# Performance work log

Measured on AMD Instinct MI355X. Metric: run time of the kernel, lower is better.

Reference implementation:

```python
import jax, jax.numpy as jnp
import numpy as np

MEM_DIM = 256
MEM_SIZE = 2048
N = 32768
K1 = 10
K2 = 10
BN_EPS = 1e-5
LEAKY_SLOPE = 0.01


def setup_inputs() -> dict:
    key = jax.random.key(0)
    k_x, k_m1, k_m2 = jax.random.split(key, 3)
    stdv = 1.0 / np.sqrt(MEM_DIM)
    x = jax.random.normal(k_x, (N, MEM_DIM), dtype=jnp.float32)
    mem1 = jax.random.uniform(k_m1, (MEM_SIZE, MEM_DIM), dtype=jnp.float32, minval=-stdv, maxval=stdv)
    mem2 = jax.random.uniform(k_m2, (MEM_SIZE, MEM_DIM), dtype=jnp.float32, minval=-stdv, maxval=stdv)
    gamma1 = jnp.ones((MEM_DIM,), jnp.float32)
    beta1 = jnp.zeros((MEM_DIM,), jnp.float32)
    gamma2 = jnp.ones((MEM_DIM,), jnp.float32)
    beta2 = jnp.zeros((MEM_DIM,), jnp.float32)
    return {"x": x, "mem1": mem1, "mem2": mem2,
            "gamma1": gamma1, "beta1": beta1, "gamma2": gamma2, "beta2": beta2}


def _basic_unit(x, mem, k):
    # cosine similarity: (x @ M^T) / (||x|| * ||M||)  -> [N, mem_size]
    sim = (x @ mem.T) / (jnp.linalg.norm(x, axis=1, keepdims=True)
                         * jnp.linalg.norm(mem, axis=1)[None, :])
    S, I = jax.lax.top_k(sim, k)                      # [N, k]
    w = jax.nn.softmax(jax.nn.relu(S), axis=1)        # sparse addressing weights
    # gather memory rows and weighted-sum: einsum('abc,ab->ac')
    return jnp.einsum('nkd,nk->nd', mem[I], w)


def _batchnorm_train(x, gamma, beta):
    mu = jnp.mean(x, axis=0)
    var = jnp.var(x, axis=0)  # biased, as torch BatchNorm uses for normalization
    return gamma * (x - mu) / jnp.sqrt(var + BN_EPS) + beta


def _leaky_relu(x):
    return jnp.where(x >= 0, x, LEAKY_SLOPE * x)


def reference(x, mem1, mem2, gamma1, beta1, gamma2, beta2):
    h = _basic_unit(x, mem1, K1)
    h = _leaky_relu(_batchnorm_train(h, gamma1, beta1))
    h = _basic_unit(h, mem2, K2)
    h = _leaky_relu(_batchnorm_train(h, gamma2, beta2))
    return h
```

## Files before the change

kernel.cpp:

```cpp
#include <hip/hip_runtime.h>
#include <math.h>


#define NROWS 32768
#define DIM   256
#define MSIZE 2048
#define TK    10
#define BM    64
#define BN    256
#define KC    32
#define NKC   8
#define NCC   8
#define NTHR  512
#define BNEPS 1e-5f
#define SLOPE 0.01f

union UMem {
  float ms[2][KC][BN];
  struct {
    float tw[8][8][TK];
    int   tx[8][8][TK];
    float cs[8][BN];
    float cq[8][BN];
  } f;
};

#define INSERT(LI, V, XI)                                               \
  do {                                                                  \
    const float v_ = (V);                                               \
    if (v_ > tv[LI][TK-1]) {                                            \
      float t_ = v_; int x_ = (XI);                                     \
      _Pragma("unroll")                                                 \
      for (int p_ = 0; p_ < TK; ++p_) {                                 \
        const bool  sw_ = (t_ > tv[LI][p_]);                            \
        const float ov_ = tv[LI][p_]; const int ox_ = ti_[LI][p_];      \
        tv[LI][p_]  = sw_ ? t_ : ov_;  ti_[LI][p_] = sw_ ? x_ : ox_;    \
        t_ = sw_ ? ov_ : t_;  x_ = sw_ ? ox_ : x_;                      \
      }                                                                 \
    }                                                                   \
  } while (0)

__global__ void __launch_bounds__(NTHR, 1) unit_kernel(
    const float* __restrict__ X,
    const float* __restrict__ M,
    const float* __restrict__ Minv,
    float* __restrict__ H,
    float* __restrict__ csum, float* __restrict__ csq)
{
  __shared__ float xs[BM][DIM];
  __shared__ UMem u;

  const int  tid  = threadIdx.x;
  const int  w    = tid >> 6;
  const int  lane = tid & 63;
  const bool hi   = lane >= 32;
  const int  row0 = blockIdx.x * BM;

  #pragma unroll
  for (int p = 0; p < 8; ++p) {
    const int r = p * 8 + w;
    const float4 v = reinterpret_cast<const float4*>(X + (size_t)(row0 + r) * DIM)[lane];
    float s = v.x*v.x + v.y*v.y + v.z*v.z + v.w*v.w;
    #pragma unroll
    for (int m = 32; m >= 1; m >>= 1) s += __shfl_xor(s, m, 64);
    const float sc = 1.0f / sqrtf(s);
    const float4 o = {v.x*sc, v.y*sc, v.z*sc, v.w*sc};
    reinterpret_cast<float4*>(&xs[r][0])[lane] = o;
  }
  __syncthreads();

  float tv[4][TK]; int ti_[4][TK];
  #pragma unroll
  for (int i = 0; i < 4; ++i)
    #pragma unroll
    for (int p = 0; p < TK; ++p) { tv[i][p] = -INFINITY; ti_[i][p] = 0x7FFFFFFF; }

  const int kq = tid & 7;

  for (int cc = 0; cc < NCC; ++cc) {
    const int col0 = cc * BN;

    float mc[4]; const float4* msrc[4]; int sloc[4];
    #pragma unroll
    for (int p = 0; p < 4; ++p) {
      const int mloc = p * 64 + (tid >> 3);
      mc[p]   = Minv[col0 + mloc];
      msrc[p] = reinterpret_cast<const float4*>(M + (size_t)(col0 + mloc) * DIM) + kq;
      sloc[p] = mloc ^ (kq << 3);
    }

    float acc[8][4];
    #pragma unroll
    for (int i = 0; i < 8; ++i)
      #pragma unroll
      for (int j = 0; j < 4; ++j) acc[i][j] = 0.f;

    float4 g[4];
    #pragma unroll
    for (int p = 0; p < 4; ++p) g[p] = msrc[p][0];
    #pragma unroll
    for (int p = 0; p < 4; ++p) {
      u.ms[0][kq*4+0][sloc[p]] = g[p].x * mc[p];
      u.ms[0][kq*4+1][sloc[p]] = g[p].y * mc[p];
      u.ms[0][kq*4+2][sloc[p]] = g[p].z * mc[p];
      u.ms[0][kq*4+3][sloc[p]] = g[p].w * mc[p];
    }
    __syncthreads();

    for (int kc = 0; kc < NKC; ++kc) {
      const int cur = kc & 1;
      if (kc < NKC - 1) {
        #pragma unroll
        for (int p = 0; p < 4; ++p) g[p] = msrc[p][(kc + 1) * 8];
      }
      #pragma unroll
      for (int k4 = 0; k4 < KC/4; ++k4) {
        float4 a4[8];
        #pragma unroll
        for (int i = 0; i < 8; ++i)
          a4[i] = *reinterpret_cast<const float4*>(&xs[w*8 + i][kc*KC + k4*4]);
        const int bcol = (lane * 4) ^ (k4 << 3);
        #pragma unroll
        for (int j4 = 0; j4 < 4; ++j4) {
          const float4 b = *reinterpret_cast<const float4*>(&u.ms[cur][k4*4 + j4][bcol]);
          #pragma unroll
          for (int i = 0; i < 8; ++i) {
            const float a = reinterpret_cast<const float*>(&a4[i])[j4];
            acc[i][0] = fmaf(a, b.x, acc[i][0]);
            acc[i][1] = fmaf(a, b.y, acc[i][1]);
            acc[i][2] = fmaf(a, b.z, acc[i][2]);
            acc[i][3] = fmaf(a, b.w, acc[i][3]);
          }
        }
      }
      if (kc < NKC - 1) {
        const int nxt = cur ^ 1;
        #pragma unroll
        for (int p = 0; p < 4; ++p) {
          u.ms[nxt][kq*4+0][sloc[p]] = g[p].x * mc[p];
          u.ms[nxt][kq*4+1][sloc[p]] = g[p].y * mc[p];
          u.ms[nxt][kq*4+2][sloc[p]] = g[p].z * mc[p];
          u.ms[nxt][kq*4+3][sloc[p]] = g[p].w * mc[p];
        }
        __syncthreads();
      }
    }

    float gv[4][4];
    #pragma unroll
    for (int i = 0; i < 4; ++i)
      #pragma unroll
      for (int j = 0; j < 4; ++j) {
        const float give = hi ? acc[i][j] : acc[i+4][j];
        gv[i][j] = __shfl_xor(give, 32, 64);
      }
    const int ownc = col0 + lane * 4;
    const int gotc = col0 + (lane ^ 32) * 4;
    #pragma unroll
    for (int i = 0; i < 4; ++i) {
      #pragma unroll
      for (int j = 0; j < 4; ++j) {
        const float v = hi ? gv[i][j] : acc[i][j];
        INSERT(i, v, (hi ? gotc : ownc) + j);
      }
      #pragma unroll
      for (int j = 0; j < 4; ++j) {
        const float v = hi ? acc[i+4][j] : gv[i][j];
        INSERT(i, v, (hi ? ownc : gotc) + j);
      }
    }
  }
  __syncthreads();

  #pragma unroll
  for (int li = 0; li < 4; ++li) {
    float wv[TK]; int wx[TK];
    #pragma unroll
    for (int e = 0; e < TK; ++e) {
      float hv = tv[li][0]; int hx = ti_[li][0];
      #pragma unroll
      for (int m = 1; m <= 16; m <<= 1) {
        const float ov = __shfl_xor(hv, m, 64);
        const int   ox = __shfl_xor(hx, m, 64);
        const bool take = (ov > hv) || ((ov == hv) && (ox < hx));
        hv = take ? ov : hv; hx = take ? ox : hx;
      }
      wv[e] = hv; wx[e] = hx;
      if (ti_[li][0] == hx) {
        #pragma unroll
        for (int p = 0; p < TK-1; ++p) { tv[li][p] = tv[li][p+1]; ti_[li][p] = ti_[li][p+1]; }
        tv[li][TK-1] = -INFINITY; ti_[li][TK-1] = 0x7FFFFFFF;
      }
    }
    const float mx = fmaxf(wv[0], 0.f);
    float we[TK]; float ssum = 0.f;
    #pragma unroll
    for (int e = 0; e < TK; ++e) { we[e] = expf(fmaxf(wv[e], 0.f) - mx); ssum += we[e]; }
    const float winv = 1.0f / ssum;
    const int r8 = (hi ? 4 : 0) + li;
    if ((lane & 31) == 0) {
      #pragma unroll
      for (int e = 0; e < TK; ++e) { u.f.tw[w][r8][e] = we[e] * winv; u.f.tx[w][r8][e] = wx[e]; }
    }
  }
  __syncthreads();

  float cS[4] = {0,0,0,0}, cQ[4] = {0,0,0,0};
  #pragma unroll
  for (int r8 = 0; r8 < 8; ++r8) {
    float h0 = 0.f, h1 = 0.f, h2 = 0.f, h3 = 0.f;
    #pragma unroll
    for (int e = 0; e < TK; ++e) {
      const float we = u.f.tw[w][r8][e];
      const int   xe = u.f.tx[w][r8][e];
      const float4 mv = reinterpret_cast<const float4*>(M + (size_t)xe * DIM)[lane];
      h0 = fmaf(we, mv.x, h0); h1 = fmaf(we, mv.y, h1);
      h2 = fmaf(we, mv.z, h2); h3 = fmaf(we, mv.w, h3);
    }
    const int row = row0 + w*8 + r8;
    const float4 o = {h0, h1, h2, h3};
    reinterpret_cast<float4*>(H + (size_t)row * DIM)[lane] = o;
    cS[0] += h0; cS[1] += h1; cS[2] += h2; cS[3] += h3;
    cQ[0] = fmaf(h0,h0,cQ[0]); cQ[1] = fmaf(h1,h1,cQ[1]);
    cQ[2] = fmaf(h2,h2,cQ[2]); cQ[3] = fmaf(h3,h3,cQ[3]);
  }
  {
    const float4 s4 = {cS[0],cS[1],cS[2],cS[3]}, q4 = {cQ[0],cQ[1],cQ[2],cQ[3]};
    *reinterpret_cast<float4*>(&u.f.cs[w][lane*4]) = s4;
    *reinterpret_cast<float4*>(&u.f.cq[w][lane*4]) = q4;
  }
  __syncthreads();
  {
    const int col = tid & 255;
    float s = 0.f;
    if (tid < 256) {
      #pragma unroll
      for (int w8 = 0; w8 < 8; ++w8) s += u.f.cs[w8][col];
      atomicAdd(&csum[col], s);
    } else {
      #pragma unroll
      for (int w8 = 0; w8 < 8; ++w8) s += u.f.cq[w8][col];
      atomicAdd(&csq[col], s);
    }
  }
}

__global__ void __launch_bounds__(256) memnorm_kernel(
    const float* __restrict__ m1, const float* __restrict__ m2,
    float* __restrict__ inv1, float* __restrict__ inv2)
{
  const int row  = blockIdx.x * 4 + (threadIdx.x >> 6);
  const int lane = threadIdx.x & 63;
  const float* src = (row < MSIZE) ? m1 : m2;
  const int r = row & (MSIZE - 1);
  const float4 v = reinterpret_cast<const float4*>(src)[r * (DIM/4) + lane];
  float s = v.x*v.x + v.y*v.y + v.z*v.z + v.w*v.w;
  #pragma unroll
  for (int m = 32; m >= 1; m >>= 1) s += __shfl_xor(s, m, 64);
  if (lane == 0) ((row < MSIZE) ? inv1 : inv2)[r] = 1.0f / sqrtf(s);
}

__global__ void __launch_bounds__(256) bn_kernel(
    const float* __restrict__ in, float* __restrict__ out,
    const float* __restrict__ cs, const float* __restrict__ cq,
    const float* __restrict__ gam, const float* __restrict__ bet)
{
  const int tid = threadIdx.x;
  const int c0  = (tid & 63) * 4;
  const int ro  = tid >> 6;
  const float invN = 1.0f / (float)NROWS;
  float sc[4], sh[4];
  #pragma unroll
  for (int j = 0; j < 4; ++j) {
    const int c = c0 + j;
    const float mean = cs[c] * invN;
    const float var  = cq[c] * invN - mean * mean;
    const float s    = gam[c] / sqrtf(var + BNEPS);
    sc[j] = s; sh[j] = bet[c] - mean * s;
  }
  const int rbase = blockIdx.x * 128;
  #pragma unroll 4
  for (int it = 0; it < 32; ++it) {
    const int r = rbase + ro + it * 4;
    const float4 v = reinterpret_cast<const float4*>(in + (size_t)r * DIM)[tid & 63];
    float y0 = fmaf(sc[0], v.x, sh[0]);
    float y1 = fmaf(sc[1], v.y, sh[1]);
    float y2 = fmaf(sc[2], v.z, sh[2]);
    float y3 = fmaf(sc[3], v.w, sh[3]);
    y0 = y0 >= 0.f ? y0 : SLOPE * y0;
    y1 = y1 >= 0.f ? y1 : SLOPE * y1;
    y2 = y2 >= 0.f ? y2 : SLOPE * y2;
    y3 = y3 >= 0.f ? y3 : SLOPE * y3;
    const float4 o = {y0, y1, y2, y3};
    reinterpret_cast<float4*>(out + (size_t)r * DIM)[tid & 63] = o;
  }
}

extern "C" void kernel_launch(void* const* d_in, const int* in_sizes, int n_in,
                              void* d_out, int out_size, void* d_ws, size_t ws_size,
                              hipStream_t stream) {
  (void)in_sizes; (void)n_in; (void)out_size; (void)ws_size;
  const float* x    = (const float*)d_in[0];
  const float* mem1 = (const float*)d_in[1];
  const float* mem2 = (const float*)d_in[2];
  const float* g1   = (const float*)d_in[3];
  const float* b1   = (const float*)d_in[4];
  const float* g2   = (const float*)d_in[5];
  const float* b2   = (const float*)d_in[6];
  float* out = (float*)d_out;
  float* ws  = (float*)d_ws;

  float* minv1 = ws;
  float* minv2 = ws + 2048;
  float* cs1   = ws + 4096;
  float* cq1   = ws + 4352;
  float* cs2   = ws + 4608;
  float* cq2   = ws + 4864;

  memnorm_kernel<<<(2 * MSIZE) / 4, 256, 0, stream>>>(mem1, mem2, minv1, minv2);
  hipMemsetAsync(cs1, 0, 4 * 256 * sizeof(float), stream);

  unit_kernel<<<NROWS / BM, NTHR, 0, stream>>>(x, mem1, minv1, out, cs1, cq1);
  bn_kernel<<<NROWS / 128, 256, 0, stream>>>(out, out, cs1, cq1, g1, b1);
  unit_kernel<<<NROWS / BM, NTHR, 0, stream>>>(out, mem2, minv2, out, cs2, cq2);
  bn_kernel<<<NROWS / 128, 256, 0, stream>>>(out, out, cs2, cq2, g2, b2);
}
```

Baseline: 8.697 ms.

## Move BN stats out of unit kernel and target two waves per EU

Removes the per-block column sum and sum-of-squares reduction and its global atomics from the unit kernel, and replaces them with separate partial-sum and reduce kernels over the output. The unit kernel now uses amdgpu_waves_per_eu(2,2) in place of launch_bounds min-blocks 1, and its register-array loops are rewritten as explicit float4 scalars to help allocation. The intent is to cut LDS use and register pressure so two blocks can share a CU, at the cost of an extra full read of H and two extra launches per layer. Forcing two waves per EU may make the compiler spill registers.

```diff
diff --git a/kernel.cpp b/kernel.cpp
--- a/kernel.cpp
+++ b/kernel.cpp
@@ -12,6 +12,7 @@
 #define NKC   8
 #define NCC   8
 #define NTHR  512
+#define SBLK  128
 #define BNEPS 1e-5f
 #define SLOPE 0.01f
 
@@ -20,8 +21,6 @@
   struct {
     float tw[8][8][TK];
     int   tx[8][8][TK];
-    float cs[8][BN];
-    float cq[8][BN];
   } f;
 };
 
@@ -36,16 +35,34 @@
         const float ov_ = tv[LI][p_]; const int ox_ = ti_[LI][p_];      \
         tv[LI][p_]  = sw_ ? t_ : ov_;  ti_[LI][p_] = sw_ ? x_ : ox_;    \
         t_ = sw_ ? ov_ : t_;  x_ = sw_ ? ox_ : x_;                      \
-      }                                                                 \
+      }                                                                  \
     }                                                                   \
   } while (0)
 
-__global__ void __launch_bounds__(NTHR, 1) unit_kernel(
+#define FMA_ROW(ACC, AV)                                                \
+  ACC.x = fmaf((AV), b.x, ACC.x); ACC.y = fmaf((AV), b.y, ACC.y);       \
+  ACC.z = fmaf((AV), b.z, ACC.z); ACC.w = fmaf((AV), b.w, ACC.w);
+
+#define K4STEP(J4, COMP)                                                \
+  { const float4 b = *reinterpret_cast<const float4*>(&u.ms[cur][k4*4 + (J4)][bcol]); \
+    FMA_ROW(acc0, a_0.COMP) FMA_ROW(acc1, a_1.COMP)                     \
+    FMA_ROW(acc2, a_2.COMP) FMA_ROW(acc3, a_3.COMP)                     \
+    FMA_ROW(acc4, a_4.COMP) FMA_ROW(acc5, a_5.COMP)                     \
+    FMA_ROW(acc6, a_6.COMP) FMA_ROW(acc7, a_7.COMP) }
+
+#define STAGE1(BUF, G, MC, SL)                                          \
+  u.ms[BUF][kq*4+0][SL] = (G).x * (MC);                                 \
+  u.ms[BUF][kq*4+1][SL] = (G).y * (MC);                                 \
+  u.ms[BUF][kq*4+2][SL] = (G).z * (MC);                                 \
+  u.ms[BUF][kq*4+3][SL] = (G).w * (MC);
+
+__global__ void __launch_bounds__(NTHR)
+__attribute__((amdgpu_waves_per_eu(2, 2)))
+unit_kernel(
     const float* __restrict__ X,
     const float* __restrict__ M,
     const float* __restrict__ Minv,
-    float* __restrict__ H,
-    float* __restrict__ csum, float* __restrict__ csq)
+    float* __restrict__ H)
 {
   __shared__ float xs[BM][DIM];
   __shared__ UMem u;
@@ -75,100 +92,89 @@
     #pragma unroll
     for (int p = 0; p < TK; ++p) { tv[i][p] = -INFINITY; ti_[i][p] = 0x7FFFFFFF; }
 
-  const int kq = tid & 7;
+  const int kq   = tid & 7;
+  const int mrow = tid >> 3;
+  const int sl   = mrow ^ (kq << 3);
+  const int sloc0 = sl, sloc1 = 64 + sl, sloc2 = 128 + sl, sloc3 = 192 + sl;
 
   for (int cc = 0; cc < NCC; ++cc) {
     const int col0 = cc * BN;
 
-    float mc[4]; const float4* msrc[4]; int sloc[4];
-    #pragma unroll
-    for (int p = 0; p < 4; ++p) {
-      const int mloc = p * 64 + (tid >> 3);
-      mc[p]   = Minv[col0 + mloc];
-      msrc[p] = reinterpret_cast<const float4*>(M + (size_t)(col0 + mloc) * DIM) + kq;
-      sloc[p] = mloc ^ (kq << 3);
-    }
-
-    float acc[8][4];
-    #pragma unroll
-    for (int i = 0; i < 8; ++i)
-      #pragma unroll
-      for (int j = 0; j < 4; ++j) acc[i][j] = 0.f;
-
-    float4 g[4];
-    #pragma unroll
-    for (int p = 0; p < 4; ++p) g[p] = msrc[p][0];
-    #pragma unroll
-    for (int p = 0; p < 4; ++p) {
-      u.ms[0][kq*4+0][sloc[p]] = g[p].x * mc[p];
-      u.ms[0][kq*4+1][sloc[p]] = g[p].y * mc[p];
-      u.ms[0][kq*4+2][sloc[p]] = g[p].z * mc[p];
-      u.ms[0][kq*4+3][sloc[p]] = g[p].w * mc[p];
-    }
+    const float mc0 = Minv[col0 + mrow];
+    const float mc1 = Minv[col0 + 64 + mrow];
+    const float mc2 = Minv[col0 + 128 + mrow];
+    const float mc3 = Minv[col0 + 192 + mrow];
+    const float4* msrc0 = reinterpret_cast<const float4*>(M + (size_t)(col0 +        mrow) * DIM) + kq;
+    const float4* msrc1 = reinterpret_cast<const float4*>(M + (size_t)(col0 +  64 + mrow) * DIM) + kq;
+    const float4* msrc2 = reinterpret_cast<const float4*>(M + (size_t)(col0 + 128 + mrow) * DIM) + kq;
+    const float4* msrc3 = reinterpret_cast<const float4*>(M + (size_t)(col0 + 192 + mrow) * DIM) + kq;
+
+    float4 acc0 = {0,0,0,0}, acc1 = {0,0,0,0}, acc2 = {0,0,0,0}, acc3 = {0,0,0,0};
+    float4 acc4 = {0,0,0,0}, acc5 = {0,0,0,0}, acc6 = {0,0,0,0}, acc7 = {0,0,0,0};
+
+    float4 g0 = msrc0[0], g1 = msrc1[0], g2 = msrc2[0], g3 = msrc3[0];
+    STAGE1(0, g0, mc0, sloc0) STAGE1(0, g1, mc1, sloc1)
+    STAGE1(0, g2, mc2, sloc2) STAGE1(0, g3, mc3, sloc3)
     __syncthreads();
 
     for (int kc = 0; kc < NKC; ++kc) {
       const int cur = kc & 1;
       if (kc < NKC - 1) {
-        #pragma unroll
-        for (int p = 0; p < 4; ++p) g[p] = msrc[p][(kc + 1) * 8];
+        g0 = msrc0[(kc + 1) * 8]; g1 = msrc1[(kc + 1) * 8];
+        g2 = msrc2[(kc + 1) * 8]; g3 = msrc3[(kc + 1) * 8];
       }
       #pragma unroll
       for (int k4 = 0; k4 < KC/4; ++k4) {
-        float4 a4[8];
-        #pragma unroll
-        for (int i = 0; i < 8; ++i)
-          a4[i] = *reinterpret_cast<const float4*>(&xs[w*8 + i][kc*KC + k4*4]);
+        const int kbase = kc * KC + k4 * 4;
+        const float4 a_0 = *reinterpret_cast<const float4*>(&xs[w*8 + 0][kbase]);
+        const float4 a_1 = *reinterpret_cast<const float4*>(&xs[w*8 + 1][kbase]);
+        const float4 a_2 = *reinterpret_cast<const float4*>(&xs[w*8 + 2][kbase]);
+        const float4 a_3 = *reinterpret_cast<const float4*>(&xs[w*8 + 3][kbase]);
+        const float4 a_4 = *reinterpret_cast<const float4*>(&xs[w*8 + 4][kbase]);
+        const float4 a_5 = *reinterpret_cast<const float4*>(&xs[w*8 + 5][kbase]);
+        const float4 a_6 = *reinterpret_cast<const float4*>(&xs[w*8 + 6][kbase]);
+        const float4 a_7 = *reinterpret_cast<const float4*>(&xs[w*8 + 7][kbase]);
         const int bcol = (lane * 4) ^ (k4 << 3);
-        #pragma unroll
-        for (int j4 = 0; j4 < 4; ++j4) {
-          const float4 b = *reinterpret_cast<const float4*>(&u.ms[cur][k4*4 + j4][bcol]);
-          #pragma unroll
-          for (int i = 0; i < 8; ++i) {
-            const float a = reinterpret_cast<const float*>(&a4[i])[j4];
-            acc[i][0] = fmaf(a, b.x, acc[i][0]);
-            acc[i][1] = fmaf(a, b.y, acc[i][1]);
-            acc[i][2] = fmaf(a, b.z, acc[i][2]);
-            acc[i][3] = fmaf(a, b.w, acc[i][3]);
-          }
-        }
+        K4STEP(0, x) K4STEP(1, y) K4STEP(2, z) K4STEP(3, w)
       }
       if (kc < NKC - 1) {
         const int nxt = cur ^ 1;
-        #pragma unroll
-        for (int p = 0; p < 4; ++p) {
-          u.ms[nxt][kq*4+0][sloc[p]] = g[p].x * mc[p];
-          u.ms[nxt][kq*4+1][sloc[p]] = g[p].y * mc[p];
-          u.ms[nxt][kq*4+2][sloc[p]] = g[p].z * mc[p];
-          u.ms[nxt][kq*4+3][sloc[p]] = g[p].w * mc[p];
-        }
+        STAGE1(nxt, g0, mc0, sloc0) STAGE1(nxt, g1, mc1, sloc1)
+        STAGE1(nxt, g2, mc2, sloc2) STAGE1(nxt, g3, mc3, sloc3)
         __syncthreads();
       }
     }
 
-    float gv[4][4];
-    #pragma unroll
-    for (int i = 0; i < 4; ++i)
-      #pragma unroll
-      for (int j = 0; j < 4; ++j) {
-        const float give = hi ? acc[i][j] : acc[i+4][j];
-        gv[i][j] = __shfl_xor(give, 32, 64);
-      }
+    float4 gv0, gv1, gv2, gv3;
+    {
+      const float4 s0 = hi ? acc0 : acc4;
+      const float4 s1 = hi ? acc1 : acc5;
+      const float4 s2 = hi ? acc2 : acc6;
+      const float4 s3 = hi ? acc3 : acc7;
+      gv0.x = __shfl_xor(s0.x, 32, 64); gv0.y = __shfl_xor(s0.y, 32, 64);
+      gv0.z = __shfl_xor(s0.z, 32, 64); gv0.w = __shfl_xor(s0.w, 32, 64);
+      gv1.x = __shfl_xor(s1.x, 32, 64); gv1.y = __shfl_xor(s1.y, 32, 64);
+      gv1.z = __shfl_xor(s1.z, 32, 64); gv1.w = __shfl_xor(s1.w, 32, 64);
+      gv2.x = __shfl_xor(s2.x, 32, 64); gv2.y = __shfl_xor(s2.y, 32, 64);
+      gv2.z = __shfl_xor(s2.z, 32, 64); gv2.w = __shfl_xor(s2.w, 32, 64);
+      gv3.x = __shfl_xor(s3.x, 32, 64); gv3.y = __shfl_xor(s3.y, 32, 64);
+      gv3.z = __shfl_xor(s3.z, 32, 64); gv3.w = __shfl_xor(s3.w, 32, 64);
+    }
     const int ownc = col0 + lane * 4;
     const int gotc = col0 + (lane ^ 32) * 4;
-    #pragma unroll
-    for (int i = 0; i < 4; ++i) {
-      #pragma unroll
-      for (int j = 0; j < 4; ++j) {
-        const float v = hi ? gv[i][j] : acc[i][j];
-        INSERT(i, v, (hi ? gotc : ownc) + j);
-      }
-      #pragma unroll
-      for (int j = 0; j < 4; ++j) {
-        const float v = hi ? acc[i+4][j] : gv[i][j];
-        INSERT(i, v, (hi ? ownc : gotc) + j);
-      }
-    }
+    const int cA = hi ? gotc : ownc;
+    const int cB = hi ? ownc : gotc;
+    #define INS_LIST(LI, GVI, AI, AI4)                                   \
+      { const float4 fb = hi ? (GVI) : (AI); const float4 sb = hi ? (AI4) : (GVI); \
+        INSERT(LI, fb.x, cA+0); INSERT(LI, fb.y, cA+1);                  \
+        INSERT(LI, fb.z, cA+2); INSERT(LI, fb.w, cA+3);                  \
+        INSERT(LI, sb.x, cB+0); INSERT(LI, sb.y, cB+1);                  \
+        INSERT(LI, sb.z, cB+2); INSERT(LI, sb.w, cB+3); }
+    INS_LIST(0, gv0, acc0, acc4)
+    INS_LIST(1, gv1, acc1, acc5)
+    INS_LIST(2, gv2, acc2, acc6)
+    INS_LIST(3, gv3, acc3, acc7)
+    #undef INS_LIST
   }
   __syncthreads();
 
@@ -205,7 +211,6 @@
   }
   __syncthreads();
 
-  float cS[4] = {0,0,0,0}, cQ[4] = {0,0,0,0};
   #pragma unroll
   for (int r8 = 0; r8 < 8; ++r8) {
     float h0 = 0.f, h1 = 0.f, h2 = 0.f, h3 = 0.f;
@@ -220,28 +225,6 @@
     const int row = row0 + w*8 + r8;
     const float4 o = {h0, h1, h2, h3};
     reinterpret_cast<float4*>(H + (size_t)row * DIM)[lane] = o;
-    cS[0] += h0; cS[1] += h1; cS[2] += h2; cS[3] += h3;
-    cQ[0] = fmaf(h0,h0,cQ[0]); cQ[1] = fmaf(h1,h1,cQ[1]);
-    cQ[2] = fmaf(h2,h2,cQ[2]); cQ[3] = fmaf(h3,h3,cQ[3]);
-  }
-  {
-    const float4 s4 = {cS[0],cS[1],cS[2],cS[3]}, q4 = {cQ[0],cQ[1],cQ[2],cQ[3]};
-    *reinterpret_cast<float4*>(&u.f.cs[w][lane*4]) = s4;
-    *reinterpret_cast<float4*>(&u.f.cq[w][lane*4]) = q4;
-  }
-  __syncthreads();
-  {
-    const int col = tid & 255;
-    float s = 0.f;
-    if (tid < 256) {
-      #pragma unroll
-      for (int w8 = 0; w8 < 8; ++w8) s += u.f.cs[w8][col];
-      atomicAdd(&csum[col], s);
-    } else {
-      #pragma unroll
-      for (int w8 = 0; w8 < 8; ++w8) s += u.f.cq[w8][col];
-      atomicAdd(&csq[col], s);
-    }
   }
 }
 
@@ -258,6 +241,36 @@
   #pragma unroll
   for (int m = 32; m >= 1; m >>= 1) s += __shfl_xor(s, m, 64);
   if (lane == 0) ((row < MSIZE) ? inv1 : inv2)[r] = 1.0f / sqrtf(s);
+}
+
+__global__ void __launch_bounds__(256) stats_part_kernel(
+    const float* __restrict__ H, float* __restrict__ part)
+{
+  const int c = threadIdx.x;
+  const int b = blockIdx.x;
+  const int rows = NROWS / SBLK;
+  const float* p = H + (size_t)b * rows * DIM + c;
+  float s = 0.f, q = 0.f;
+  #pragma unroll 8
+  for (int r = 0; r < rows; ++r) {
+    const float v = p[(size_t)r * DIM];
+    s += v; q = fmaf(v, v, q);
+  }
+  part[(size_t)(b * 2 + 0) * DIM + c] = s;
+  part[(size_t)(b * 2 + 1) * DIM + c] = q;
+}
+
+__global__ void __launch_bounds__(512) stats_reduce_kernel(
+    const float* __restrict__ part, float* __restrict__ cs, float* __restrict__ cq)
+{
+  const int t  = threadIdx.x;
+  const int c  = t & 255;
+  const int sq = t >> 8;
+  float s = 0.f;
+  #pragma unroll 8
+  for (int b = 0; b < SBLK; ++b)
+    s += part[(size_t)(b * 2 + sq) * DIM + c];
+  (sq ? cq : cs)[c] = s;
 }
 
 __global__ void __launch_bounds__(256) bn_kernel(
@@ -312,16 +325,21 @@
 
   float* minv1 = ws;
   float* minv2 = ws + 2048;
-  float* cs1   = ws + 4096;
-  float* cq1   = ws + 4352;
-  float* cs2   = ws + 4608;
-  float* cq2   = ws + 4864;
+  float* part  = ws + 4096;
+  float* cs1   = ws + 4096 + SBLK * 2 * DIM;
+  float* cq1   = cs1 + 256;
+  float* cs2   = cq1 + 256;
+  float* cq2   = cs2 + 256;
 
   memnorm_kernel<<<(2 * MSIZE) / 4, 256, 0, stream>>>(mem1, mem2, minv1, minv2);
-  hipMemsetAsync(cs1, 0, 4 * 256 * sizeof(float), stream);
-
-  unit_kernel<<<NROWS / BM, NTHR, 0, stream>>>(x, mem1, minv1, out, cs1, cq1);
+
+  unit_kernel<<<NROWS / BM, NTHR, 0, stream>>>(x, mem1, minv1, out);
+  stats_part_kernel<<<SBLK, 256, 0, stream>>>(out, part);
+  stats_reduce_kernel<<<1, 512, 0, stream>>>(part, cs1, cq1);
   bn_kernel<<<NROWS / 128, 256, 0, stream>>>(out, out, cs1, cq1, g1, b1);
-  unit_kernel<<<NROWS / BM, NTHR, 0, stream>>>(out, mem2, minv2, out, cs2, cq2);
+
+  unit_kernel<<<NROWS / BM, NTHR, 0, stream>>>(out, mem2, minv2, out);
+  stats_part_kernel<<<SBLK, 256, 0, stream>>>(out, part);
+  stats_reduce_kernel<<<1, 512, 0, stream>>>(part, cs2, cq2);
   bn_kernel<<<NROWS / 128, 256, 0, stream>>>(out, out, cs2, cq2, g2, b2);
 }
```

Result: slower. 9.353 ms (+7.6%).
